# Performance work log

Measured on AMD Instinct MI355X. Metric: run time of the kernel, lower is better.

## Reference

```python
import jax, jax.numpy as jnp
import numpy as np

D_MODEL = 1024
N_HEAD = 16
DIM_PER_HEAD = D_MODEL // N_HEAD
B, S = 8, 1024


def setup_inputs() -> dict:
    key = jax.random.key(0)
    ks = jax.random.split(key, 12)
    s = 0.02
    return {
        "k": jax.random.normal(ks[0], (B, S, D_MODEL), jnp.float32),
        "v": jax.random.normal(ks[1], (B, S, D_MODEL), jnp.float32),
        "q": jax.random.normal(ks[2], (B, S, D_MODEL), jnp.float32),
        "attn_mask": jax.random.randint(ks[3], (B, S, S), 0, 2, jnp.int32),
        "Wk": jax.random.normal(ks[4], (D_MODEL, D_MODEL), jnp.float32) * s,
        "bk": jnp.zeros((D_MODEL,), jnp.float32),
        "Wv": jax.random.normal(ks[5], (D_MODEL, D_MODEL), jnp.float32) * s,
        "bv": jnp.zeros((D_MODEL,), jnp.float32),
        "Wq": jax.random.normal(ks[6], (D_MODEL, D_MODEL), jnp.float32) * s,
        "bq": jnp.zeros((D_MODEL,), jnp.float32),
        "Wo": jax.random.normal(ks[7], (D_MODEL, D_MODEL), jnp.float32) * s,
        "bo": jnp.zeros((D_MODEL,), jnp.float32),
    }


def reference(k, v, q, attn_mask, Wk, bk, Wv, bv, Wq, bq, Wo, bo):
    batch, key_len, _ = k.shape
    query_len = q.shape[1]
    scale = 1.0 / jnp.sqrt(jnp.float32(DIM_PER_HEAD))

    def split_heads(x):  # [b, s, d] -> [b, h, s, dh]
        return x.reshape(batch, -1, N_HEAD, DIM_PER_HEAD).transpose(0, 2, 1, 3)

    key_up = split_heads(k @ Wk + bk)
    value_up = split_heads(v @ Wv + bv)
    query_up = split_heads(q @ Wq + bq) * scale

    # [b, h, q, k] scores; mask nonzero entries with -inf (masked_fill_ semantics)
    scores = jnp.einsum("bhqd,bhkd->bhqk", query_up, key_up)
    scores = jnp.where(attn_mask[:, None, :, :] != 0, -jnp.inf, scores)
    attn = jax.nn.softmax(scores, axis=-1)
    # NOTE: original applies dropout but discards the result; attn (pre-dropout) is used.
    context = jnp.einsum("bhqk,bhkd->bhqd", attn, value_up)
    context = context.transpose(0, 2, 1, 3).reshape(batch, query_len, D_MODEL)
    output = context @ Wo + bo
    attn_mean = attn.sum(axis=1) / N_HEAD  # [b, q, k]
    return output, attn_mean
```

## Files before the change

kernel.cpp:

```cpp
#include <hip/hip_runtime.h>
#include <hip/hip_bf16.h>

typedef unsigned short u16;
typedef unsigned int u32;
typedef __attribute__((ext_vector_type(8))) short bf16x8;
typedef __attribute__((ext_vector_type(4))) float f32x4;
typedef __attribute__((ext_vector_type(4))) u16 u16x4;

#define DEV static __device__ __forceinline__

DEV u16 f2bf(float x) {
  unsigned u = __builtin_bit_cast(unsigned, x);
  u += 0x7fffu + ((u >> 16) & 1u);
  return (u16)(u >> 16);
}
DEV float bf2f(u16 u) { return __builtin_bit_cast(float, ((unsigned)u) << 16); }

DEV void glds16(const u16* g, u16* l) {
  __builtin_amdgcn_global_load_lds(
      (const __attribute__((address_space(1))) void*)g,
      (__attribute__((address_space(3))) void*)l, 16, 0, 0);
}

__global__ __launch_bounds__(256) void xcvt(
    const float* __restrict__ k, const float* __restrict__ v,
    const float* __restrict__ q, u16* __restrict__ Xb) {
  const size_t i0 = (size_t)blockIdx.x * 256 + threadIdx.x;
  for (size_t t = i0; t < 6291456; t += 524288) {
    const size_t e = t * 4;
    const float* src = (e < 8388608) ? k + e
                     : (e < 16777216) ? v + (e - 8388608)
                     : q + (e - 16777216);
    const f32x4 x = *(const f32x4*)src;
    u16x4 o;
#pragma unroll
    for (int r = 0; r < 4; ++r) o[r] = f2bf(x[r]);
    *(u16x4*)&Xb[e] = o;
  }
}

__global__ __launch_bounds__(256) void transpose_w(
    const float* __restrict__ w0, const float* __restrict__ w1,
    const float* __restrict__ w2, const float* __restrict__ w3,
    u16* __restrict__ out) {
  __shared__ u16 tile[32][33];
  const int mat = blockIdx.y;
  const float* in = (mat == 0) ? w0 : (mat == 1) ? w1 : (mat == 2) ? w2 : w3;
  u16* o = out + (size_t)mat * 1048576;
  const int bk = ((int)blockIdx.x & 31) << 5;
  const int bn = ((int)blockIdx.x >> 5) << 5;
  const int tx = threadIdx.x & 31, ty = threadIdx.x >> 5;
#pragma unroll
  for (int i = 0; i < 32; i += 8)
    tile[ty + i][tx] = f2bf(in[(size_t)(bk + ty + i) * 1024 + bn + tx]);
  __syncthreads();
#pragma unroll
  for (int i = 0; i < 32; i += 8)
    o[(size_t)(bn + ty + i) * 1024 + bk + tx] = tile[tx][ty + i];
}

__global__ __launch_bounds__(256) void gemm_qkv(
    const u16* __restrict__ Xb, const u16* __restrict__ WTall,
    const float* __restrict__ bK, const float* __restrict__ bV,
    const float* __restrict__ bQ,
    u16* __restrict__ Kup, u16* __restrict__ VupT, u16* __restrict__ Qup) {
  __shared__ u16 As[4096];
  __shared__ u16 Bs[4096];
  const int mode = blockIdx.y;
  const u16* A = Xb + (size_t)mode * 8388608;
  const u16* Bw = WTall + (size_t)mode * 1048576;
  const float* bias = (mode == 0) ? bK : (mode == 1) ? bV : bQ;

  const int tid = threadIdx.x;
  const int w = tid >> 6, l = tid & 63;
  const int ln = l & 15, lg = l >> 4, kg8 = lg << 3;
  const int wr = w >> 1, wc = w & 1;
  const int mb = ((int)blockIdx.x >> 3) << 7;
  const int nb = ((int)blockIdx.x & 7) << 7;

  const int srow = (w << 5) + (l >> 2);
  const int sseg = (l & 3) << 3;
  const u16* Ag0 = A + (size_t)(mb + srow) * 1024 + sseg;
  const u16* Bg0 = Bw + (size_t)(nb + srow) * 1024 + sseg;
  u16* Al0 = As + srow * 32 + sseg;
  u16* Bl0 = Bs + srow * 32 + sseg;

  f32x4 acc[4][4] = {};
  const int ar = (wr << 6) + ln;
  const int br = (wc << 6) + ln;

  for (int k0 = 0; k0 < 1024; k0 += 32) {
    glds16(Ag0 + k0, Al0);
    glds16(Ag0 + 16384 + k0, Al0 + 512);
    glds16(Bg0 + k0, Bl0);
    glds16(Bg0 + 16384 + k0, Bl0 + 512);
    __syncthreads();
    bf16x8 aa[4], bb[4];
#pragma unroll
    for (int mt = 0; mt < 4; ++mt) aa[mt] = *(const bf16x8*)&As[(ar + (mt << 4)) * 32 + kg8];
#pragma unroll
    for (int nt = 0; nt < 4; ++nt) bb[nt] = *(const bf16x8*)&Bs[(br + (nt << 4)) * 32 + kg8];
#pragma unroll
    for (int mt = 0; mt < 4; ++mt)
#pragma unroll
      for (int nt = 0; nt < 4; ++nt)
        acc[mt][nt] = __builtin_amdgcn_mfma_f32_16x16x32_bf16(aa[mt], bb[nt], acc[mt][nt], 0, 0, 0);
    __syncthreads();
  }

  const float scale = (mode == 2) ? 0.125f : 1.0f;
#pragma unroll
  for (int mt = 0; mt < 4; ++mt) {
    const int m0 = mb + (wr << 6) + (mt << 4) + (lg << 2);
    const int bb_ = m0 >> 10, s0 = m0 & 1023;
#pragma unroll
    for (int nt = 0; nt < 4; ++nt) {
      const int n = nb + (wc << 6) + (nt << 4) + ln;
      const float bval = bias[n];
      const int h = n >> 6, dh = n & 63;
      const size_t bh = (size_t)(bb_ * 16 + h);
      if (mode == 1) {
        const int wv = dh >> 4, lnv = dh & 15;
        const int kk = s0 >> 5, lgv = (s0 >> 3) & 3, e0 = s0 & 7;
        u16x4 pk;
#pragma unroll
        for (int r = 0; r < 4; ++r) pk[r] = f2bf(acc[mt][nt][r] + bval);
        *(u16x4*)&VupT[(bh << 16) + (wv << 14) + (kk << 9) + (lgv << 7) +
                       (lnv << 3) + e0] = pk;
      } else if (mode == 0) {
        const int half = dh >> 5, lg2 = (dh >> 3) & 3, e = dh & 7;
        const int T = s0 >> 4;
        u16* base = Kup + (bh << 16) + (T << 10) + (half << 9) + (lg2 << 7) + e;
#pragma unroll
        for (int r = 0; r < 4; ++r)
          base[((s0 & 15) + r) << 3] = f2bf(acc[mt][nt][r] + bval);
      } else {
#pragma unroll
        for (int r = 0; r < 4; ++r)
          Qup[((bh << 10) + s0 + r) * 64 + dh] =
              f2bf((acc[mt][nt][r] + bval) * scale);
      }
    }
  }
}

__global__ __launch_bounds__(256) void gemm_out(
    const u16* __restrict__ Ctx, const u16* __restrict__ WTall,
    const float* __restrict__ bO, float* __restrict__ Out) {
  __shared__ u16 As[4096];
  __shared__ u16 Bs[4096];
  const u16* Bw = WTall + 3145728;

  const int tid = threadIdx.x;
  const int w = tid >> 6, l = tid & 63;
  const int ln = l & 15, lg = l >> 4, kg8 = lg << 3;
  const int wr = w >> 1, wc = w & 1;
  const int mb = ((int)blockIdx.x >> 3) << 7;
  const int nb = ((int)blockIdx.x & 7) << 7;

  const int srow = (w << 5) + (l >> 2);
  const int sseg = (l & 3) << 3;
  const u16* Ag0 = Ctx + (size_t)(mb + srow) * 1024 + sseg;
  const u16* Bg0 = Bw + (size_t)(nb + srow) * 1024 + sseg;
  u16* Al0 = As + srow * 32 + sseg;
  u16* Bl0 = Bs + srow * 32 + sseg;

  f32x4 acc[4][4] = {};
  const int ar = (wr << 6) + ln;
  const int br = (wc << 6) + ln;

  for (int k0 = 0; k0 < 1024; k0 += 32) {
    glds16(Ag0 + k0, Al0);
    glds16(Ag0 + 16384 + k0, Al0 + 512);
    glds16(Bg0 + k0, Bl0);
    glds16(Bg0 + 16384 + k0, Bl0 + 512);
    __syncthreads();
    bf16x8 aa[4], bb[4];
#pragma unroll
    for (int mt = 0; mt < 4; ++mt) aa[mt] = *(const bf16x8*)&As[(ar + (mt << 4)) * 32 + kg8];
#pragma unroll
    for (int nt = 0; nt < 4; ++nt) bb[nt] = *(const bf16x8*)&Bs[(br + (nt << 4)) * 32 + kg8];
#pragma unroll
    for (int mt = 0; mt < 4; ++mt)
#pragma unroll
      for (int nt = 0; nt < 4; ++nt)
        acc[mt][nt] = __builtin_amdgcn_mfma_f32_16x16x32_bf16(aa[mt], bb[nt], acc[mt][nt], 0, 0, 0);
    __syncthreads();
  }
#pragma unroll
  for (int mt = 0; mt < 4; ++mt) {
    const int m0 = mb + (wr << 6) + (mt << 4) + (lg << 2);
#pragma unroll
    for (int nt = 0; nt < 4; ++nt) {
      const int n = nb + (wc << 6) + (nt << 4) + ln;
      const float bval = bO[n];
#pragma unroll
      for (int r = 0; r < 4; ++r)
        Out[(size_t)(m0 + r) * 1024 + n] = acc[mt][nt][r] + bval;
    }
  }
}

__global__ __launch_bounds__(256, 2) void attn_kernel(
    const u16* __restrict__ Qup, const u16* __restrict__ Kf,
    const u16* __restrict__ Vf, const int* __restrict__ mask,
    u16* __restrict__ Ctx, u16* __restrict__ Pp) {
  __shared__ u16 P_lds[16 * 1024];
  __shared__ float red_s[4][16];
  __shared__ float invs[16];

  const int tid = threadIdx.x;
  const int w = tid >> 6, l = tid & 63;
  const int ln = l & 15, lg = l >> 4;
  const int kg8 = lg << 3;

  const int bid = (int)blockIdx.x;
  const int swz = ((bid & 7) << 9) | (bid >> 3);
  const int qb = (swz & 63) << 4;
  const int b = (swz >> 6) & 7;
  const int hs = swz >> 9;

  const int* Mp = mask + ((size_t)b << 20) + ((size_t)qb << 10);
  unsigned long long mbits = 0ull;
#pragma unroll
  for (int t = 0; t < 16; ++t) {
    const int key = (w << 8) + (t << 4) + ln;
#pragma unroll
    for (int r = 0; r < 4; ++r) {
      const int row = (lg << 2) + r;
      if (Mp[((size_t)row << 10) + key] != 0) mbits |= 1ull << ((t << 2) + r);
    }
  }

  bf16x8 accv[8];

#pragma unroll 1
  for (int hh = 0; hh < 2; ++hh) {
    const int h = (hs << 1) + hh;
    const size_t bh = (size_t)(b * 16 + h);
    const u16* Qp = Qup + ((bh << 10) + qb) * 64;
    const u16* Kb = Kf + (bh << 16);
    const u16* Vb = Vf + (bh << 16) + ((size_t)w << 14);

    const bf16x8 qa0 = *(const bf16x8*)&Qp[ln * 64 + kg8];
    const bf16x8 qa1 = *(const bf16x8*)&Qp[ln * 64 + 32 + kg8];

    bf16x8 ka[3], kb[3];
#pragma unroll
    for (int p = 0; p < 3; ++p) {
      const int To = ((w << 4) + p) << 10;
      ka[p] = *(const bf16x8*)&Kb[To + (l << 3)];
      kb[p] = *(const bf16x8*)&Kb[To + 512 + (l << 3)];
    }

    float rsum[4] = {0, 0, 0, 0};
#pragma unroll
    for (int t = 0; t < 16; ++t) {
      const int s = t % 3;
      const bf16x8 k0 = ka[s], k1 = kb[s];
      if (t + 3 < 16) {
        const int To = ((w << 4) + t + 3) << 10;
        ka[s] = *(const bf16x8*)&Kb[To + (l << 3)];
        kb[s] = *(const bf16x8*)&Kb[To + 512 + (l << 3)];
      }
      f32x4 c = {0, 0, 0, 0};
      c = __builtin_amdgcn_mfma_f32_16x16x32_bf16(qa0, k0, c, 0, 0, 0);
      c = __builtin_amdgcn_mfma_f32_16x16x32_bf16(qa1, k1, c, 0, 0, 0);
      const int key = (w << 8) + (t << 4) + ln;
#pragma unroll
      for (int r = 0; r < 4; ++r) {
        const float p =
            ((mbits >> ((t << 2) + r)) & 1ull) ? 0.0f : __expf(c[r] - 4.0f);
        rsum[r] += p;
        const int row = (lg << 2) + r;
        const int bo_ = ((row << 11) + (key << 1)) ^ ((row & 7) << 4);
        *(u16*)((char*)P_lds + bo_) = f2bf(p);
      }
    }
#pragma unroll
    for (int off = 1; off < 16; off <<= 1) {
#pragma unroll
      for (int r = 0; r < 4; ++r) rsum[r] += __shfl_xor(rsum[r], off);
    }
    if (ln == 0) {
#pragma unroll
      for (int r = 0; r < 4; ++r) red_s[w][(lg << 2) + r] = rsum[r];
    }

    bf16x8 vr[4];
#pragma unroll
    for (int p = 0; p < 4; ++p)
      vr[p] = *(const bf16x8*)&Vb[(p << 9) + (l << 3)];

    __syncthreads();
    float inv[4];
#pragma unroll
    for (int r = 0; r < 4; ++r) {
      const int row = (lg << 2) + r;
      inv[r] = 1.0f / (red_s[0][row] + red_s[1][row] + red_s[2][row] + red_s[3][row]);
    }
    if (ln == 0) {
#pragma unroll
      for (int r = 0; r < 4; ++r) invs[(lg << 2) + r] = inv[r];
    }

    f32x4 c0 = {0, 0, 0, 0}, c1 = {0, 0, 0, 0};
#pragma unroll
    for (int kk = 0; kk < 32; ++kk) {
      const int s = kk & 3;
      const bf16x8 vb = vr[s];
      if (kk + 4 < 32)
        vr[s] = *(const bf16x8*)&Vb[((kk + 4) << 9) + (l << 3)];
      const int a0 = ((ln << 11) + (((kk << 5) + kg8) << 1)) ^ ((ln & 7) << 4);
      const bf16x8 pa = *(const bf16x8*)((const char*)P_lds + a0);
      if (kk & 1)
        c1 = __builtin_amdgcn_mfma_f32_16x16x32_bf16(pa, vb, c1, 0, 0, 0);
      else
        c0 = __builtin_amdgcn_mfma_f32_16x16x32_bf16(pa, vb, c0, 0, 0, 0);
    }
#pragma unroll
    for (int r = 0; r < 4; ++r) {
      const int row = (lg << 2) + r;
      Ctx[(((size_t)b << 10) + qb + row) * 1024 + (h << 6) + (w << 4) + ln] =
          f2bf((c0[r] + c1[r]) * inv[r]);
    }

    {
      const int row = tid >> 4;
      const float iv = invs[row];
      u16* Pg = Pp + ((size_t)hs << 23) + (((size_t)b << 10) + qb + row) * 1024;
#pragma unroll
      for (int i = 0; i < 8; ++i) {
        const int chunk = (tid & 15) + (i << 4);
        const int bo_ = ((row << 11) + (chunk << 4)) ^ ((row & 7) << 4);
        const bf16x8 pv = *(const bf16x8*)((const char*)P_lds + bo_);
        if (hh == 0) {
          bf16x8 o;
#pragma unroll
          for (int e = 0; e < 8; ++e) o[e] = (short)f2bf(bf2f((u16)pv[e]) * iv);
          accv[i] = o;
        } else {
          bf16x8 o;
#pragma unroll
          for (int e = 0; e < 8; ++e)
            o[e] = (short)f2bf(bf2f((u16)accv[i][e]) + bf2f((u16)pv[e]) * iv);
          *(bf16x8*)&Pg[chunk << 3] = o;
        }
      }
    }
    __syncthreads();
  }
}

__global__ __launch_bounds__(256) void combine(
    const u16* __restrict__ Pp, float* __restrict__ Am) {
  const size_t i = ((size_t)blockIdx.x * 256 + threadIdx.x) * 8;
  float s[8] = {0, 0, 0, 0, 0, 0, 0, 0};
#pragma unroll
  for (int p = 0; p < 8; ++p) {
    const u16x4* q = (const u16x4*)&Pp[(size_t)p * 8388608 + i];
    const u16x4 a = q[0], c = q[1];
#pragma unroll
    for (int r = 0; r < 4; ++r) { s[r] += bf2f(a[r]); s[r + 4] += bf2f(c[r]); }
  }
  f32x4 lo, hi;
#pragma unroll
  for (int r = 0; r < 4; ++r) { lo[r] = s[r] * 0.0625f; hi[r] = s[r + 4] * 0.0625f; }
  *(f32x4*)&Am[i] = lo;
  *(f32x4*)&Am[i + 4] = hi;
}

extern "C" void kernel_launch(void* const* d_in, const int* in_sizes, int n_in,
                              void* d_out, int out_size, void* d_ws, size_t ws_size,
                              hipStream_t stream) {
  const float* k_in = (const float*)d_in[0];
  const float* v_in = (const float*)d_in[1];
  const float* q_in = (const float*)d_in[2];
  const int* mask = (const int*)d_in[3];
  const float* Wk = (const float*)d_in[4];
  const float* bk = (const float*)d_in[5];
  const float* Wv = (const float*)d_in[6];
  const float* bv = (const float*)d_in[7];
  const float* Wq = (const float*)d_in[8];
  const float* bq = (const float*)d_in[9];
  const float* Wo = (const float*)d_in[10];
  const float* bo = (const float*)d_in[11];

  float* out = (float*)d_out;
  float* amean = out + (size_t)8 * 1024 * 1024;

  u16* ws = (u16*)d_ws;
  u16* WT = ws;
  u16* Xb = ws + 4194304;
  u16* Pp = ws + 4194304;
  u16* Kf   = ws + 71303168;
  u16* Vf   = ws + 79691776;
  u16* Qup  = ws + 88080384;
  u16* Ctx  = ws + 96468992;

  xcvt<<<2048, 256, 0, stream>>>(k_in, v_in, q_in, Xb);
  transpose_w<<<dim3(1024, 4), dim3(256), 0, stream>>>(Wk, Wv, Wq, Wo, WT);
  gemm_qkv<<<dim3(512, 3), dim3(256), 0, stream>>>(
      Xb, WT, bk, bv, bq, Kf, Vf, Qup);
  attn_kernel<<<dim3(4096), dim3(256), 0, stream>>>(
      Qup, Kf, Vf, mask, Ctx, Pp);
  combine<<<4096, 256, 0, stream>>>(Pp, amean);
  gemm_out<<<512, 256, 0, stream>>>(Ctx, WT, bo, out);
}
```

Measured before the change: 339.8 us.

## Prepack attention mask into bitmasks once and use packed bf16 conversions

```diff
diff --git a/kernel.cpp b/kernel.cpp
--- a/kernel.cpp
+++ b/kernel.cpp
@@ -6,6 +6,7 @@
 typedef __attribute__((ext_vector_type(8))) short bf16x8;
 typedef __attribute__((ext_vector_type(4))) float f32x4;
 typedef __attribute__((ext_vector_type(4))) u16 u16x4;
+typedef __attribute__((ext_vector_type(4))) u32 u32x4;
 
 #define DEV static __device__ __forceinline__
 
@@ -15,6 +16,12 @@
   return (u16)(u >> 16);
 }
 DEV float bf2f(u16 u) { return __builtin_bit_cast(float, ((unsigned)u) << 16); }
+
+DEV u32 cvtpk(float lo, float hi) {
+  u32 r;
+  asm("v_cvt_pk_bf16_f32 %0, %1, %2" : "=v"(r) : "v"(lo), "v"(hi));
+  return r;
+}
 
 DEV void glds16(const u16* g, u16* l) {
   __builtin_amdgcn_global_load_lds(
@@ -59,6 +66,26 @@
     o[(size_t)(bn + ty + i) * 1024 + bk + tx] = tile[tx][ty + i];
 }
 
+__global__ __launch_bounds__(256) void maskpack(
+    const int* __restrict__ mask, unsigned long long* __restrict__ Mb) {
+  const int qt = blockIdx.x, b = blockIdx.y;
+  const int tid = threadIdx.x;
+  const int w = tid >> 6, l = tid & 63;
+  const int ln = l & 15, lg = l >> 4;
+  const int* Mp = mask + ((size_t)b << 20) + ((size_t)(qt << 4) << 10);
+  unsigned long long m = 0ull;
+#pragma unroll
+  for (int t = 0; t < 16; ++t) {
+    const int key = (w << 8) + (t << 4) + ln;
+#pragma unroll
+    for (int r = 0; r < 4; ++r) {
+      const int row = (lg << 2) + r;
+      if (Mp[((size_t)row << 10) + key] != 0) m |= 1ull << ((t << 2) + r);
+    }
+  }
+  Mb[((((size_t)b << 6) + qt) << 8) + tid] = m;
+}
+
 __global__ __launch_bounds__(256) void gemm_qkv(
     const u16* __restrict__ Xb, const u16* __restrict__ WTall,
     const float* __restrict__ bK, const float* __restrict__ bV,
@@ -203,7 +230,7 @@
 
 __global__ __launch_bounds__(256, 2) void attn_kernel(
     const u16* __restrict__ Qup, const u16* __restrict__ Kf,
-    const u16* __restrict__ Vf, const int* __restrict__ mask,
+    const u16* __restrict__ Vf, const unsigned long long* __restrict__ Mb,
     u16* __restrict__ Ctx, u16* __restrict__ Pp) {
   __shared__ u16 P_lds[16 * 1024];
   __shared__ float red_s[4][16];
@@ -216,23 +243,14 @@
 
   const int bid = (int)blockIdx.x;
   const int swz = ((bid & 7) << 9) | (bid >> 3);
-  const int qb = (swz & 63) << 4;
+  const int qt = swz & 63;
+  const int qb = qt << 4;
   const int b = (swz >> 6) & 7;
   const int hs = swz >> 9;
 
-  const int* Mp = mask + ((size_t)b << 20) + ((size_t)qb << 10);
-  unsigned long long mbits = 0ull;
-#pragma unroll
-  for (int t = 0; t < 16; ++t) {
-    const int key = (w << 8) + (t << 4) + ln;
-#pragma unroll
-    for (int r = 0; r < 4; ++r) {
-      const int row = (lg << 2) + r;
-      if (Mp[((size_t)row << 10) + key] != 0) mbits |= 1ull << ((t << 2) + r);
-    }
-  }
-
-  bf16x8 accv[8];
+  const unsigned long long mbits = Mb[((((size_t)b << 6) + qt) << 8) + tid];
+
+  u32x4 accp[8];
 
 #pragma unroll 1
   for (int hh = 0; hh < 2; ++hh) {
@@ -267,15 +285,19 @@
       c = __builtin_amdgcn_mfma_f32_16x16x32_bf16(qa0, k0, c, 0, 0, 0);
       c = __builtin_amdgcn_mfma_f32_16x16x32_bf16(qa1, k1, c, 0, 0, 0);
       const int key = (w << 8) + (t << 4) + ln;
+      float p[4];
 #pragma unroll
       for (int r = 0; r < 4; ++r) {
-        const float p =
-            ((mbits >> ((t << 2) + r)) & 1ull) ? 0.0f : __expf(c[r] - 4.0f);
-        rsum[r] += p;
-        const int row = (lg << 2) + r;
-        const int bo_ = ((row << 11) + (key << 1)) ^ ((row & 7) << 4);
-        *(u16*)((char*)P_lds + bo_) = f2bf(p);
+        p[r] = ((mbits >> ((t << 2) + r)) & 1ull) ? 0.0f : __expf(c[r] - 4.0f);
+        rsum[r] += p[r];
       }
+      const u32 pk01 = cvtpk(p[0], p[1]);
+      const u32 pk23 = cvtpk(p[2], p[3]);
+      const int r0 = lg << 2;
+      *(u16*)((char*)P_lds + ((((r0 + 0) << 11) + (key << 1)) ^ (((r0 + 0) & 7) << 4))) = (u16)pk01;
+      *(u16*)((char*)P_lds + ((((r0 + 1) << 11) + (key << 1)) ^ (((r0 + 1) & 7) << 4))) = (u16)(pk01 >> 16);
+      *(u16*)((char*)P_lds + ((((r0 + 2) << 11) + (key << 1)) ^ (((r0 + 2) & 7) << 4))) = (u16)pk23;
+      *(u16*)((char*)P_lds + ((((r0 + 3) << 11) + (key << 1)) ^ (((r0 + 3) & 7) << 4))) = (u16)(pk23 >> 16);
     }
 #pragma unroll
     for (int off = 1; off < 16; off <<= 1) {
@@ -318,11 +340,14 @@
       else
         c0 = __builtin_amdgcn_mfma_f32_16x16x32_bf16(pa, vb, c0, 0, 0, 0);
     }
-#pragma unroll
-    for (int r = 0; r < 4; ++r) {
-      const int row = (lg << 2) + r;
-      Ctx[(((size_t)b << 10) + qb + row) * 1024 + (h << 6) + (w << 4) + ln] =
-          f2bf((c0[r] + c1[r]) * inv[r]);
+    {
+      const u32 q01 = cvtpk((c0[0] + c1[0]) * inv[0], (c0[1] + c1[1]) * inv[1]);
+      const u32 q23 = cvtpk((c0[2] + c1[2]) * inv[2], (c0[3] + c1[3]) * inv[3]);
+      u16* Cp = &Ctx[(((size_t)b << 10) + qb + (lg << 2)) * 1024 + (h << 6) + (w << 4) + ln];
+      Cp[0] = (u16)q01;
+      Cp[1024] = (u16)(q01 >> 16);
+      Cp[2048] = (u16)q23;
+      Cp[3072] = (u16)(q23 >> 16);
     }
 
     {
@@ -333,19 +358,23 @@
       for (int i = 0; i < 8; ++i) {
         const int chunk = (tid & 15) + (i << 4);
         const int bo_ = ((row << 11) + (chunk << 4)) ^ ((row & 7) << 4);
-        const bf16x8 pv = *(const bf16x8*)((const char*)P_lds + bo_);
-        if (hh == 0) {
-          bf16x8 o;
-#pragma unroll
-          for (int e = 0; e < 8; ++e) o[e] = (short)f2bf(bf2f((u16)pv[e]) * iv);
-          accv[i] = o;
-        } else {
-          bf16x8 o;
-#pragma unroll
-          for (int e = 0; e < 8; ++e)
-            o[e] = (short)f2bf(bf2f((u16)accv[i][e]) + bf2f((u16)pv[e]) * iv);
-          *(bf16x8*)&Pg[chunk << 3] = o;
+        const u32x4 pu = *(const u32x4*)((const char*)P_lds + bo_);
+        u32x4 o;
+#pragma unroll
+        for (int j = 0; j < 4; ++j) {
+          const float plo = __builtin_bit_cast(float, pu[j] << 16) * iv;
+          const float phi = __builtin_bit_cast(float, pu[j] & 0xFFFF0000u) * iv;
+          if (hh == 0) {
+            o[j] = cvtpk(plo, phi);
+          } else {
+            const u32 a = accp[i][j];
+            const float alo = __builtin_bit_cast(float, a << 16);
+            const float ahi = __builtin_bit_cast(float, a & 0xFFFF0000u);
+            o[j] = cvtpk(alo + plo, ahi + phi);
+          }
         }
+        if (hh == 0) accp[i] = o;
+        else *(u32x4*)&Pg[chunk << 3] = o;
       }
     }
     __syncthreads();
@@ -389,6 +418,8 @@
   float* out = (float*)d_out;
   float* amean = out + (size_t)8 * 1024 * 1024;
 
+  unsigned long long* Mb = (unsigned long long*)amean;
+
   u16* ws = (u16*)d_ws;
   u16* WT = ws;
   u16* Xb = ws + 4194304;
@@ -400,10 +431,11 @@
 
   xcvt<<<2048, 256, 0, stream>>>(k_in, v_in, q_in, Xb);
   transpose_w<<<dim3(1024, 4), dim3(256), 0, stream>>>(Wk, Wv, Wq, Wo, WT);
+  maskpack<<<dim3(64, 8), dim3(256), 0, stream>>>(mask, Mb);
   gemm_qkv<<<dim3(512, 3), dim3(256), 0, stream>>>(
       Xb, WT, bk, bv, bq, Kf, Vf, Qup);
   attn_kernel<<<dim3(4096), dim3(256), 0, stream>>>(
-      Qup, Kf, Vf, mask, Ctx, Pp);
+      Qup, Kf, Vf, Mb, Ctx, Pp);
   combine<<<4096, 256, 0, stream>>>(Pp, amean);
   gemm_out<<<512, 256, 0, stream>>>(Ctx, WT, bo, out);
 }
```

Result: faster. 311.9 us (-8.2%).
